# Optimization experiments

Measured on AMD Instinct MI355X. Metric: run time of the kernel, lower is better.

The kernel has to match this reference:

```python
import jax, jax.numpy as jnp
import numpy as np

H = 128  # hidden_dim


def gcn_conv(x, src, dst, n, W, b):
    """PyG GCNConv: add self-loops, symmetric norm, gather-transform-scatter."""
    h = x @ W  # [n, H]
    loop = jnp.arange(n, dtype=src.dtype)
    s = jnp.concatenate([src, loop])
    d = jnp.concatenate([dst, loop])
    deg = jax.ops.segment_sum(jnp.ones(s.shape[0], h.dtype), d, num_segments=n)
    dinv = jnp.where(deg > 0, jax.lax.rsqrt(deg), 0.0)
    norm = dinv[s] * dinv[d]  # [E+n]
    msg = h[s] * norm[:, None]
    out = jax.ops.segment_sum(msg, d, num_segments=n)
    return out + b


def encode(x, edge_index, batch, num_graphs, params):
    src, dst = edge_index[0], edge_index[1]
    n = x.shape[0]
    for (W, b) in params:
        x = jax.nn.relu(gcn_conv(x, src, dst, n, W, b))
    sums = jax.ops.segment_sum(x, batch, num_segments=num_graphs)
    cnts = jax.ops.segment_sum(jnp.ones((n, 1), x.dtype), batch, num_segments=num_graphs)
    return sums / jnp.maximum(cnts, 1.0)  # global_mean_pool -> [B, H]


def setup_inputs() -> dict:
    key = jax.random.key(0)
    ks = jax.random.split(key, 32)
    B, C = 32, 5
    Nd, Ed = 1280, 5120
    Np, Ep = 12800, 204800
    f32 = jnp.float32

    def lin(k, fan_in, fan_out):
        k1, k2 = jax.random.split(k)
        lim = 1.0 / np.sqrt(fan_in)
        W = jax.random.uniform(k1, (fan_in, fan_out), f32, -lim, lim)
        b = jax.random.uniform(k2, (fan_out,), f32, -lim, lim)
        return W, b

    Wd0, bd0 = lin(ks[0], 78, H)
    Wd1, bd1 = lin(ks[1], H, H)
    Wd2, bd2 = lin(ks[2], H, H)
    Wp0, bp0 = lin(ks[3], 1280, H)
    Wp1, bp1 = lin(ks[4], H, H)
    Wp2, bp2 = lin(ks[5], H, H)
    Wq, bq = lin(ks[6], H, H)
    Wk, bk = lin(ks[7], H, H)
    Wv, bv = lin(ks[8], H, H)
    W1, b1 = lin(ks[9], 2 * H, H)
    W2, b2 = lin(ks[10], H, 1)

    drug_x = jax.random.normal(ks[11], (Nd, 78), f32)
    prot_x = jax.random.normal(ks[12], (C, Np, 1280), f32)
    drug_edge_index = jax.random.randint(ks[13], (2, Ed), 0, Nd, jnp.int32)
    prot_edge_index = jax.random.randint(ks[14], (C, 2, Ep), 0, Np, jnp.int32)
    # equal-sized graphs per batch element -> every segment non-empty
    drug_batch = (jnp.arange(Nd, dtype=jnp.int32) * B) // Nd
    prot_batch = (jnp.arange(Np, dtype=jnp.int32) * B) // Np

    return dict(drug_x=drug_x, prot_x=prot_x,
                Wd0=Wd0, bd0=bd0, Wd1=Wd1, bd1=bd1, Wd2=Wd2, bd2=bd2,
                Wp0=Wp0, bp0=bp0, Wp1=Wp1, bp1=bp1, Wp2=Wp2, bp2=bp2,
                Wq=Wq, bq=bq, Wk=Wk, bk=bk, Wv=Wv, bv=bv,
                W1=W1, b1=b1, W2=W2, b2=b2,
                drug_edge_index=drug_edge_index, prot_edge_index=prot_edge_index,
                drug_batch=drug_batch, prot_batch=prot_batch, num_graphs=B)


def reference(drug_x, prot_x, Wd0, bd0, Wd1, bd1, Wd2, bd2,
              Wp0, bp0, Wp1, bp1, Wp2, bp2,
              Wq, bq, Wk, bk, Wv, bv, W1, b1, W2, b2,
              drug_edge_index, prot_edge_index, drug_batch, prot_batch, num_graphs):
    drug_params = [(Wd0, bd0), (Wd1, bd1), (Wd2, bd2)]
    prot_params = [(Wp0, bp0), (Wp1, bp1), (Wp2, bp2)]

    drug_emb = encode(drug_x, drug_edge_index, drug_batch, num_graphs, drug_params)  # [B,H]

    # vmap over conformations -> [C, B, H]
    conf = jax.vmap(lambda x, ei: encode(x, ei, prot_batch, num_graphs, prot_params))(
        prot_x, prot_edge_index)
    conf = jnp.transpose(conf, (1, 0, 2))  # [B, C, H]

    # drug-conditioned cross-attention over conformations
    q = drug_emb @ Wq + bq                      # [B,H]
    keys = conf @ Wk + bk                       # [B,C,H]
    vals = conf @ Wv + bv                       # [B,C,H]
    scores = jnp.einsum('bh,bch->bc', q, keys) / jnp.sqrt(jnp.asarray(H, q.dtype))
    attn = jax.nn.softmax(scores, axis=1)       # [B,C]
    protein_emb = jnp.einsum('bc,bch->bh', attn, vals)

    combined = jnp.concatenate([drug_emb, protein_emb], axis=1)  # [B,2H]
    hidden = jax.nn.relu(combined @ W1 + b1)    # dropout is identity in eval mode
    logits = (hidden @ W2 + b2)[:, 0]           # [B]
    return logits, attn
```

## Files before the change

kernel.cpp:

```cpp
#include <hip/hip_runtime.h>

#define H     128
#define BGR   32
#define NCONF 5
#define ND    1280
#define FD    78
#define ED    5120
#define NP    12800
#define FP    1280
#define EP    204800
#define MAXD  64

#define PROT_GEMM1_BLKS 1000
#define PROT_GEMM_BLKS 500
#define DRUG_GEMM1_BLKS 20
#define DRUG_GEMM_BLKS 10
#define PLACE_BLKS 4020
#define PROT_MP_BLKS 16000
#define DRUG_MP_BLKS 320

typedef unsigned short u16;
typedef unsigned int   u32;
typedef __attribute__((ext_vector_type(8))) short bf16x8;
typedef __attribute__((ext_vector_type(4))) unsigned int u32x4;
typedef __attribute__((ext_vector_type(4))) unsigned short u16x4;
typedef __attribute__((ext_vector_type(8))) unsigned short u16x8;
typedef __attribute__((ext_vector_type(4))) float f32x4;

__device__ __forceinline__ u16 f2bf(float x) {
  u32 u = __float_as_uint(x);
  u32 r = (u + 0x7FFFu + ((u >> 16) & 1u)) >> 16;
  return (u16)r;
}
__device__ __forceinline__ float bf2f(u16 h) {
  return __uint_as_float(((u32)h) << 16);
}

__device__ __forceinline__ void gload16(const void* gsrc, void* lds) {
  __builtin_amdgcn_global_load_lds(
      (const __attribute__((address_space(1))) unsigned int*)gsrc,
      (__attribute__((address_space(3))) unsigned int*)lds, 16, 0, 0);
}

__device__ __forceinline__ void cvt8(float4 p, float4 q, bf16x8& hi, bf16x8& lo) {
  float f[8] = {p.x, p.y, p.z, p.w, q.x, q.y, q.z, q.w};
  u32x4 h, l;
  #pragma unroll
  for (int j = 0; j < 4; ++j) {
    u32 u0 = __float_as_uint(f[2 * j]);
    u32 u1 = __float_as_uint(f[2 * j + 1]);
    u32 h0 = u0 & 0xFFFF0000u;
    u32 h1 = u1 & 0xFFFF0000u;
    h[j] = (h0 >> 16) | h1;
    float l0 = f[2 * j]     - __uint_as_float(h0);
    float l1 = f[2 * j + 1] - __uint_as_float(h1);
    l[j] = (__float_as_uint(l0) >> 16) | (__float_as_uint(l1) & 0xFFFF0000u);
  }
  union { u32x4 u; bf16x8 b; } ch, cl;
  ch.u = h; cl.u = l;
  hi = ch.b; lo = cl.b;
}

__device__ __forceinline__ void splitW_chunk(
    const float* __restrict__ W, u16* __restrict__ wsW, int K, int g)
{
  int step = g >> 10;
  int r = g & 1023;
  int col = r >> 3, q = r & 7;
  int u = q ^ (col & 7);
  int kc = (u & 3) * 8;
  bool lo = u >= 4;
  int k0 = step * 32 + kc;
  u16x8 o;
  #pragma unroll
  for (int j = 0; j < 8; ++j) {
    float x = W[(size_t)(k0 + j) * 128 + col];
    u16 h = f2bf(x);
    o[j] = lo ? f2bf(x - bf2f(h)) : h;
  }
  *(u16x8*)(wsW + (size_t)g * 8) = o;
}

__global__ __launch_bounds__(256) void splitW_all_k(
    const float* __restrict__ Wp0, const float* __restrict__ Wp1,
    const float* __restrict__ Wp2, const float* __restrict__ Wd1,
    const float* __restrict__ Wd2,
    u16* __restrict__ o0, u16* __restrict__ o1, u16* __restrict__ o2,
    u16* __restrict__ o3, u16* __restrict__ o4,
    int* __restrict__ deg_p, int* __restrict__ deg_d)
{
  int g = blockIdx.x * 256 + threadIdx.x;
  for (int i = g; i < NCONF * NP + ND; i += 224 * 256) {
    if (i < NCONF * NP) deg_p[i] = 0;
    else                deg_d[i - NCONF * NP] = 0;
  }
  if      (g < 40960) splitW_chunk(Wp0, o0, FP, g);
  else if (g < 45056) splitW_chunk(Wp1, o1, H, g - 40960);
  else if (g < 49152) splitW_chunk(Wp2, o2, H, g - 45056);
  else if (g < 53248) splitW_chunk(Wd1, o3, H, g - 49152);
  else if (g < 57344) splitW_chunk(Wd2, o4, H, g - 53248);
}

__device__ __forceinline__ void gemm_pipe64_body(
    char* smemRaw, const float* __restrict__ A, const u16* __restrict__ wsW,
    u16* __restrict__ Cout, int K, int blk)
{
  u16* Wlds = (u16*)smemRaw;
  const int t = threadIdx.x;
  const int wid = t >> 6, lane = t & 63;
  const int lane15 = lane & 15, lq = lane >> 4;
  const int m0 = blk * 64;
  const int NT = K >> 5;

  const float* Ar = A + (size_t)(m0 + wid * 16 + lane15) * K + lq * 8;
  const u16* sbase = wsW + (size_t)(wid * 4) * 512 + (size_t)lane * 8;

  f32x4 acc[8];
  #pragma unroll
  for (int j = 0; j < 8; ++j) acc[j] = (f32x4){0.f, 0.f, 0.f, 0.f};

  #define STAGE_W(step, buf) do {                                   \
    const u16* s_ = sbase + (size_t)(step) * 8192;                  \
    u16* d_ = &Wlds[(buf) * 8192 + wid * 2048];                     \
    gload16(s_,        d_);                                         \
    gload16(s_ + 512,  d_ + 512);                                   \
    gload16(s_ + 1024, d_ + 1024);                                  \
    gload16(s_ + 1536, d_ + 1536);                                  \
  } while (0)

  STAGE_W(0, 0);
  asm volatile("" ::: "memory");
  float4 xa0 = *(const float4*)(Ar);
  float4 xa1 = *(const float4*)(Ar + 4);
  asm volatile("" ::: "memory");
  float4 ya0 = *(const float4*)(Ar + 32);
  float4 ya1 = *(const float4*)(Ar + 36);

  #define BODY64(T, RA0, RA1) do {                                            \
    if ((T) < NT - 1) asm volatile("s_waitcnt vmcnt(2)\ns_barrier" ::: "memory"); \
    else              asm volatile("s_waitcnt vmcnt(0)\ns_barrier"  ::: "memory"); \
    if ((T) + 1 < NT) { STAGE_W((T) + 1, ((T) + 1) & 1); }                    \
    asm volatile("" ::: "memory");                                            \
    bf16x8 ah, al;                                                            \
    cvt8(RA0, RA1, ah, al);                                                   \
    if ((T) + 2 < NT) {                                                       \
      const float* p_ = Ar + (size_t)((T) + 2) * 32;                          \
      RA0 = *(const float4*)(p_); RA1 = *(const float4*)(p_ + 4);             \
    }                                                                         \
    const char* base_ = (const char*)&Wlds[((T) & 1) * 8192];                 \
    _Pragma("unroll")                                                         \
    for (int cb = 0; cb < 8; ++cb) {                                          \
      int col_ = cb * 16 + lane15;                                            \
      const char* cbp_ = base_ + col_ * 128;                                  \
      int sw_ = (col_ & 7) << 4;                                              \
      bf16x8 bh_ = *(const bf16x8*)(cbp_ + ((lq << 4) ^ sw_));                \
      bf16x8 bl_ = *(const bf16x8*)(cbp_ + (((lq | 4) << 4) ^ sw_));          \
      acc[cb] = __builtin_amdgcn_mfma_f32_16x16x32_bf16(ah, bh_, acc[cb], 0, 0, 0); \
      acc[cb] = __builtin_amdgcn_mfma_f32_16x16x32_bf16(al, bh_, acc[cb], 0, 0, 0); \
      acc[cb] = __builtin_amdgcn_mfma_f32_16x16x32_bf16(ah, bl_, acc[cb], 0, 0, 0); \
    }                                                                         \
  } while (0)

  for (int tt = 0; tt < NT; tt += 2) {
    BODY64(tt,     xa0, xa1);
    BODY64(tt + 1, ya0, ya1);
  }
  #undef BODY64
  #undef STAGE_W

  #pragma unroll
  for (int j = 0; j < 4; ++j) {
    int row = m0 + wid * 16 + lq * 4 + j;
    u16* Crow = Cout + (size_t)row * 128 + lane15;
    #pragma unroll
    for (int cb = 0; cb < 8; ++cb)
      Crow[cb * 16] = f2bf(acc[cb][j]);
  }
}

__device__ __forceinline__ void gemm_pipe_bf16A_body(
    char* smemRaw, const u16* __restrict__ A, const u16* __restrict__ wsW,
    u16* __restrict__ Cout, int K, int blk)
{
  u16* Wlds = (u16*)smemRaw;
  const int t = threadIdx.x;
  const int wid = t >> 6, lane = t & 63;
  const int lane15 = lane & 15, lq = lane >> 4;
  const int m0 = blk * 128;
  const int NT = K >> 5;

  const u16* Ar0 = A + (size_t)(m0 + wid * 32 + lane15) * K + lq * 8;
  const u16* Ar1 = Ar0 + (size_t)16 * K;
  const u16* sbase = wsW + (size_t)(wid * 4) * 512 + (size_t)lane * 8;

  f32x4 acc[2][8];
  #pragma unroll
  for (int i = 0; i < 2; ++i)
    #pragma unroll
    for (int j = 0; j < 8; ++j)
      acc[i][j] = (f32x4){0.f, 0.f, 0.f, 0.f};

  #define STAGE_W(step, buf) do {                                   \
    const u16* s_ = sbase + (size_t)(step) * 8192;                  \
    u16* d_ = &Wlds[(buf) * 8192 + wid * 2048];                     \
    gload16(s_,        d_);                                         \
    gload16(s_ + 512,  d_ + 512);                                   \
    gload16(s_ + 1024, d_ + 1024);                                  \
    gload16(s_ + 1536, d_ + 1536);                                  \
  } while (0)

  STAGE_W(0, 0);
  asm volatile("" ::: "memory");
  u16x8 xa = *(const u16x8*)(Ar0);
  u16x8 xb = *(const u16x8*)(Ar1);
  asm volatile("" ::: "memory");
  u16x8 ya = *(const u16x8*)(Ar0 + 32);
  u16x8 yb = *(const u16x8*)(Ar1 + 32);

  #define BODYB(T, RA, RB) do {                                               \
    if ((T) < NT - 1) asm volatile("s_waitcnt vmcnt(2)\ns_barrier" ::: "memory"); \
    else              asm volatile("s_waitcnt vmcnt(0)\ns_barrier"  ::: "memory"); \
    if ((T) + 1 < NT) { STAGE_W((T) + 1, ((T) + 1) & 1); }                    \
    asm volatile("" ::: "memory");                                            \
    union { u16x8 u; bf16x8 b; } ca_, cb2_;                                   \
    ca_.u = RA; cb2_.u = RB;                                                  \
    bf16x8 a0 = ca_.b, a1 = cb2_.b;                                           \
    if ((T) + 2 < NT) {                                                       \
      RA = *(const u16x8*)(Ar0 + (size_t)((T) + 2) * 32);                     \
      RB = *(const u16x8*)(Ar1 + (size_t)((T) + 2) * 32);                     \
    }                                                                         \
    const char* base_ = (const char*)&Wlds[((T) & 1) * 8192];                 \
    _Pragma("unroll")                                                         \
    for (int cb = 0; cb < 8; ++cb) {                                          \
      int col_ = cb * 16 + lane15;                                            \
      const char* cbp_ = base_ + col_ * 128;                                  \
      int sw_ = (col_ & 7) << 4;                                              \
      bf16x8 bh_ = *(const bf16x8*)(cbp_ + ((lq << 4) ^ sw_));                \
      bf16x8 bl_ = *(const bf16x8*)(cbp_ + (((lq | 4) << 4) ^ sw_));          \
      acc[0][cb] = __builtin_amdgcn_mfma_f32_16x16x32_bf16(a0, bh_, acc[0][cb], 0, 0, 0); \
      acc[0][cb] = __builtin_amdgcn_mfma_f32_16x16x32_bf16(a0, bl_, acc[0][cb], 0, 0, 0); \
      acc[1][cb] = __builtin_amdgcn_mfma_f32_16x16x32_bf16(a1, bh_, acc[1][cb], 0, 0, 0); \
      acc[1][cb] = __builtin_amdgcn_mfma_f32_16x16x32_bf16(a1, bl_, acc[1][cb], 0, 0, 0); \
    }                                                                         \
  } while (0)

  for (int tt = 0; tt < NT; tt += 2) {
    BODYB(tt,     xa, xb);
    BODYB(tt + 1, ya, yb);
  }
  #undef BODYB
  #undef STAGE_W

  #pragma unroll
  for (int rb = 0; rb < 2; ++rb) {
    #pragma unroll
    for (int j = 0; j < 4; ++j) {
      int row = m0 + wid * 32 + rb * 16 + lq * 4 + j;
      u16* Crow = Cout + (size_t)row * 128 + lane15;
      #pragma unroll
      for (int cb = 0; cb < 8; ++cb)
        Crow[cb * 16] = f2bf(acc[rb][cb][j]);
    }
  }
}

__device__ __forceinline__ void gemm_f32_body(
    char* smemRaw, const float* __restrict__ A, const float* __restrict__ W,
    u16* __restrict__ Cout, int K, int blk)
{
  float* As = (float*)smemRaw;
  float* Bs = (float*)(smemRaw + 16 * 64 * 4);
  const int t = threadIdx.x;
  const int m0 = blk * 64;
  const int colg = (t & 31) * 4;
  const int rowg = (t >> 5) * 8;
  const int rA = t >> 2;
  const int cA = (t & 3) * 4;
  const int rB = t >> 4;
  const int cB = (t & 15) * 4;

  float acc[8][4] = {};

  for (int k0 = 0; k0 < K; k0 += 16) {
    __syncthreads();
    #pragma unroll
    for (int j = 0; j < 4; ++j) {
      int kk = k0 + cA + j;
      As[(cA + j) * 64 + rA] = (kk < K) ? A[(size_t)(m0 + rA) * K + kk] : 0.0f;
    }
    {
      int kk = k0 + rB;
      if (kk < K) {
        *(float4*)&Bs[rB * 128 + cB]      = *(const float4*)(W + (size_t)kk * 128 + cB);
        *(float4*)&Bs[rB * 128 + cB + 64] = *(const float4*)(W + (size_t)kk * 128 + cB + 64);
      } else {
        *(float4*)&Bs[rB * 128 + cB]      = make_float4(0.f, 0.f, 0.f, 0.f);
        *(float4*)&Bs[rB * 128 + cB + 64] = make_float4(0.f, 0.f, 0.f, 0.f);
      }
    }
    __syncthreads();
    #pragma unroll
    for (int k = 0; k < 16; ++k) {
      float4 b  = *(const float4*)&Bs[k * 128 + colg];
      float4 a0 = *(const float4*)&As[k * 64 + rowg];
      float4 a1 = *(const float4*)&As[k * 64 + rowg + 4];
      const float av[8] = {a0.x, a0.y, a0.z, a0.w, a1.x, a1.y, a1.z, a1.w};
      #pragma unroll
      for (int i = 0; i < 8; ++i) {
        acc[i][0] += av[i] * b.x;
        acc[i][1] += av[i] * b.y;
        acc[i][2] += av[i] * b.z;
        acc[i][3] += av[i] * b.w;
      }
    }
  }
  #pragma unroll
  for (int i = 0; i < 8; ++i) {
    u16x4 o;
    o[0] = f2bf(acc[i][0]); o[1] = f2bf(acc[i][1]);
    o[2] = f2bf(acc[i][2]); o[3] = f2bf(acc[i][3]);
    *(u16x4*)(Cout + (size_t)(m0 + rowg + i) * 128 + colg) = o;
  }
}

__global__ __launch_bounds__(256, 4) void stage1_place_k(
    const float* __restrict__ pA, const u16* __restrict__ pW, u16* __restrict__ pC,
    const float* __restrict__ dA, const float* __restrict__ dW, u16* __restrict__ dC,
    const int* __restrict__ prot_ei, const int* __restrict__ drug_ei,
    int* __restrict__ deg_p, u16* __restrict__ slot_p,
    int* __restrict__ deg_d, u16* __restrict__ slot_d)
{
  __shared__ __align__(16) char smem[2 * 16384];
  int b = blockIdx.x;
  if (b < PROT_GEMM1_BLKS) {
    gemm_pipe64_body(smem, pA, pW, pC, FP, b);
    return;
  }
  b -= PROT_GEMM1_BLKS;
  if (b < DRUG_GEMM1_BLKS) {
    gemm_f32_body(smem, dA, dW, dC, FD, b);
    return;
  }
  b -= DRUG_GEMM1_BLKS;
  int idx = b * 256 + threadIdx.x;
  if (idx < NCONF * EP) {
    int c = idx / EP, e = idx - c * EP;
    const int* eic = prot_ei + (size_t)c * 2 * EP;
    int s = eic[e], d = eic[EP + e];
    int node = c * NP + d;
    int pos = atomicAdd(&deg_p[node], 1);
    if (pos < MAXD) slot_p[(size_t)node * MAXD + pos] = (u16)s;
  } else {
    idx -= NCONF * EP;
    if (idx < ED) {
      int s = drug_ei[idx], d = drug_ei[ED + idx];
      int pos = atomicAdd(&deg_d[d], 1);
      if (pos < MAXD) slot_d[(size_t)d * MAXD + pos] = (u16)s;
    }
  }
}

__global__ __launch_bounds__(256, 4) void stage23_gemm_k(
    const u16* __restrict__ pA, const u16* __restrict__ pW, u16* __restrict__ pC,
    const u16* __restrict__ dA, const u16* __restrict__ dW, u16* __restrict__ dC)
{
  __shared__ __align__(16) char smem[2 * 16384];
  if (blockIdx.x < PROT_GEMM_BLKS)
    gemm_pipe_bf16A_body(smem, pA, pW, pC, H, blockIdx.x);
  else
    gemm_pipe_bf16A_body(smem, dA, dW, dC, H, blockIdx.x - PROT_GEMM_BLKS);
}

__device__ __forceinline__ void mp_body(
    const u16* __restrict__ h, u16* __restrict__ xout,
    const int* __restrict__ deg, const u16* __restrict__ slots,
    const float* __restrict__ bias, int wid, int nPer)
{
  int lane = threadIdx.x & 63;
  int c = wid / nPer;
  const int* dg = deg + (size_t)c * nPer;
  int v = wid - c * nPer;
  const u32* hc = (const u32*)(h + (size_t)c * nPer * H);
  const u16* sl = slots + (size_t)wid * MAXD;
  int degv = dg[v];
  float dv = rsqrtf((float)degv + 1.0f);
  u32 us = ((const u32*)h)[(size_t)wid * 64 + lane];
  float a0x = __uint_as_float(us << 16) * dv;
  float a0y = __uint_as_float(us & 0xFFFF0000u) * dv;
  float a1x = 0.f, a1y = 0.f;
  int n = degv < MAXD ? degv : MAXD;
  int i = 0;
  for (; i + 4 <= n; i += 4) {
    int s0 = sl[i], s1 = sl[i + 1], s2 = sl[i + 2], s3 = sl[i + 3];
    float d0 = rsqrtf((float)dg[s0] + 1.0f);
    float d1 = rsqrtf((float)dg[s1] + 1.0f);
    float d2 = rsqrtf((float)dg[s2] + 1.0f);
    float d3 = rsqrtf((float)dg[s3] + 1.0f);
    u32 u0 = hc[(size_t)s0 * 64 + lane];
    u32 u1 = hc[(size_t)s1 * 64 + lane];
    u32 u2 = hc[(size_t)s2 * 64 + lane];
    u32 u3 = hc[(size_t)s3 * 64 + lane];
    a0x += __uint_as_float(u0 << 16) * d0;
    a0y += __uint_as_float(u0 & 0xFFFF0000u) * d0;
    a1x += __uint_as_float(u1 << 16) * d1;
    a1y += __uint_as_float(u1 & 0xFFFF0000u) * d1;
    a0x += __uint_as_float(u2 << 16) * d2;
    a0y += __uint_as_float(u2 & 0xFFFF0000u) * d2;
    a1x += __uint_as_float(u3 << 16) * d3;
    a1y += __uint_as_float(u3 & 0xFFFF0000u) * d3;
  }
  for (; i < n; ++i) {
    int s0 = sl[i];
    float d0 = rsqrtf((float)dg[s0] + 1.0f);
    u32 u0 = hc[(size_t)s0 * 64 + lane];
    a0x += __uint_as_float(u0 << 16) * d0;
    a0y += __uint_as_float(u0 & 0xFFFF0000u) * d0;
  }
  int col = lane * 2;
  float ox = fmaxf((a0x + a1x) * dv + bias[col],     0.0f);
  float oy = fmaxf((a0y + a1y) * dv + bias[col + 1], 0.0f);
  u32 ow = (u32)f2bf(ox) | ((u32)f2bf(oy) << 16);
  ((u32*)xout)[(size_t)wid * 64 + lane] = ow;
}

__global__ __launch_bounds__(256) void mp_all_k(
    const u16* __restrict__ hp, u16* __restrict__ xp,
    const int* __restrict__ degp, const u16* __restrict__ slotp,
    const float* __restrict__ biasp,
    const u16* __restrict__ hd, u16* __restrict__ xd,
    const int* __restrict__ degd, const u16* __restrict__ slotd,
    const float* __restrict__ biasd)
{
  int bid = blockIdx.x;
  int cpx = gridDim.x >> 3;
  bid = (bid & 7) * cpx + (bid >> 3);
  int wv = threadIdx.x >> 6;
  if (bid < PROT_MP_BLKS) {
    mp_body(hp, xp, degp, slotp, biasp, bid * 4 + wv, NP);
  } else {
    mp_body(hd, xd, degd, slotd, biasd, (bid - PROT_MP_BLKS) * 4 + wv, ND);
  }
}

__device__ __forceinline__ void pool_body(
    const u16* __restrict__ x, float* __restrict__ out, int blk, int npg)
{
  __shared__ float part[4][128];
  const int col = threadIdx.x & 127;
  const int rp  = threadIdx.x >> 7;
  size_t row0 = (size_t)blk * npg;
  float acc = 0.0f;
  for (int i = rp; i < npg; i += 4)
    acc += bf2f(x[(row0 + i) * H + col]);
  part[rp][col] = acc;
  __syncthreads();
  if (rp == 0)
    out[(size_t)blk * H + col] =
        (part[0][col] + part[1][col] + part[2][col] + part[3][col]) / (float)npg;
}

__global__ __launch_bounds__(512) void pool_all_k(
    const u16* __restrict__ xd, float* __restrict__ outd,
    const u16* __restrict__ xp, float* __restrict__ outp)
{
  if (blockIdx.x < BGR) pool_body(xd, outd, blockIdx.x, ND / BGR);
  else                  pool_body(xp, outp, blockIdx.x - BGR, NP / BGR);
}

__global__ __launch_bounds__(128) void attn_mlp_k(
    const float* __restrict__ drug_emb, const float* __restrict__ conf_pool,
    const float* __restrict__ Wq, const float* __restrict__ bq,
    const float* __restrict__ Wk, const float* __restrict__ bk,
    const float* __restrict__ Wv, const float* __restrict__ bv,
    const float* __restrict__ W1, const float* __restrict__ b1,
    const float* __restrict__ W2, const float* __restrict__ b2,
    float* __restrict__ out)
{
  const int b = blockIdx.x;
  const int hcol = threadIdx.x;
  __shared__ float de[H], pc[H], vals_s[NCONF][H], red[H], sc[NCONF], peS[H];

  de[hcol] = drug_emb[(size_t)b * H + hcol];
  __syncthreads();

  float qv = bq[hcol];
  for (int k = 0; k < H; ++k) qv += de[k] * Wq[k * H + hcol];

  for (int c = 0; c < NCONF; ++c) {
    __syncthreads();
    pc[hcol] = conf_pool[((size_t)c * BGR + b) * H + hcol];
    __syncthreads();
    float kk = bk[hcol], vv = bv[hcol];
    for (int k = 0; k < H; ++k) {
      float p = pc[k];
      kk += p * Wk[k * H + hcol];
      vv += p * Wv[k * H + hcol];
    }
    vals_s[c][hcol] = vv;
    red[hcol] = qv * kk;
    __syncthreads();
    for (int s = 64; s > 0; s >>= 1) {
      if (hcol < s) red[hcol] += red[hcol + s];
      __syncthreads();
    }
    if (hcol == 0) sc[c] = red[0] * 0.08838834764831845f;
  }
  __syncthreads();

  float m = sc[0];
  for (int c = 1; c < NCONF; ++c) m = fmaxf(m, sc[c]);
  float ex[NCONF], sum = 0.0f;
  for (int c = 0; c < NCONF; ++c) { ex[c] = expf(sc[c] - m); sum += ex[c]; }
  float inv = 1.0f / sum;
  if (hcol < NCONF) out[BGR + b * NCONF + hcol] = ex[hcol] * inv;

  float pe = 0.0f;
  for (int c = 0; c < NCONF; ++c) pe += (ex[c] * inv) * vals_s[c][hcol];
  peS[hcol] = pe;
  __syncthreads();

  float hid = b1[hcol];
  for (int k = 0; k < H; ++k) hid += de[k]  * W1[k * H + hcol];
  for (int k = 0; k < H; ++k) hid += peS[k] * W1[(H + k) * H + hcol];
  hid = fmaxf(hid, 0.0f);

  red[hcol] = hid * W2[hcol];
  __syncthreads();
  for (int s = 64; s > 0; s >>= 1) {
    if (hcol < s) red[hcol] += red[hcol + s];
    __syncthreads();
  }
  if (hcol == 0) out[b] = red[0] + b2[0];
}

extern "C" void kernel_launch(void* const* d_in, const int* in_sizes, int n_in,
                              void* d_out, int out_size, void* d_ws, size_t ws_size,
                              hipStream_t stream)
{
  const float* drug_x  = (const float*)d_in[0];
  const float* prot_x  = (const float*)d_in[1];
  const float* Wd0 = (const float*)d_in[2];  const float* bd0 = (const float*)d_in[3];
  const float* Wd1 = (const float*)d_in[4];  const float* bd1 = (const float*)d_in[5];
  const float* Wd2 = (const float*)d_in[6];  const float* bd2 = (const float*)d_in[7];
  const float* Wp0 = (const float*)d_in[8];  const float* bp0 = (const float*)d_in[9];
  const float* Wp1 = (const float*)d_in[10]; const float* bp1 = (const float*)d_in[11];
  const float* Wp2 = (const float*)d_in[12]; const float* bp2 = (const float*)d_in[13];
  const float* Wq  = (const float*)d_in[14]; const float* bq  = (const float*)d_in[15];
  const float* Wk  = (const float*)d_in[16]; const float* bk  = (const float*)d_in[17];
  const float* Wv  = (const float*)d_in[18]; const float* bv  = (const float*)d_in[19];
  const float* W1  = (const float*)d_in[20]; const float* b1  = (const float*)d_in[21];
  const float* W2  = (const float*)d_in[22]; const float* b2  = (const float*)d_in[23];
  const int* drug_ei = (const int*)d_in[24];
  const int* prot_ei = (const int*)d_in[25];
  float* out = (float*)d_out;

  char* base = (char*)d_ws;
  size_t off = 0;
  auto alloc = [&](size_t bytes) -> char* {
    char* p = base + off;
    off = (off + bytes + 255) & ~(size_t)255;
    return p;
  };
  int*   deg_p   = (int*)  alloc((size_t)NCONF * NP * 4);
  int*   deg_d   = (int*)  alloc((size_t)ND * 4);
  u16*   slot_p  = (u16*)  alloc((size_t)NCONF * NP * MAXD * 2);
  u16*   slot_d  = (u16*)  alloc((size_t)ND * MAXD * 2);
  u16*   bufHp   = (u16*)  alloc((size_t)NCONF * NP * H * 2);
  u16*   bufXp   = (u16*)  alloc((size_t)NCONF * NP * H * 2);
  u16*   bufHd   = (u16*)  alloc((size_t)ND * H * 2);
  u16*   bufXd   = (u16*)  alloc((size_t)ND * H * 2);
  float* drugemb = (float*)alloc((size_t)BGR * H * 4);
  float* confp   = (float*)alloc((size_t)NCONF * BGR * H * 4);
  u16* Wp0ws = (u16*)alloc((size_t)FP * 512);
  u16* Wp1ws = (u16*)alloc((size_t)H * 512);
  u16* Wp2ws = (u16*)alloc((size_t)H * 512);
  u16* Wd1ws = (u16*)alloc((size_t)H * 512);
  u16* Wd2ws = (u16*)alloc((size_t)H * 512);

  splitW_all_k<<<224, 256, 0, stream>>>(Wp0, Wp1, Wp2, Wd1, Wd2,
                                        Wp0ws, Wp1ws, Wp2ws, Wd1ws, Wd2ws,
                                        deg_p, deg_d);

  stage1_place_k<<<PROT_GEMM1_BLKS + DRUG_GEMM1_BLKS + PLACE_BLKS, 256, 0, stream>>>(
      prot_x, Wp0ws, bufHp, drug_x, Wd0, bufHd,
      prot_ei, drug_ei, deg_p, slot_p, deg_d, slot_d);

  mp_all_k<<<PROT_MP_BLKS + DRUG_MP_BLKS, 256, 0, stream>>>(
      bufHp, bufXp, deg_p, slot_p, bp0,
      bufHd, bufXd, deg_d, slot_d, bd0);
  stage23_gemm_k<<<PROT_GEMM_BLKS + DRUG_GEMM_BLKS, 256, 0, stream>>>(
      bufXp, Wp1ws, bufHp, bufXd, Wd1ws, bufHd);
  mp_all_k<<<PROT_MP_BLKS + DRUG_MP_BLKS, 256, 0, stream>>>(
      bufHp, bufXp, deg_p, slot_p, bp1,
      bufHd, bufXd, deg_d, slot_d, bd1);
  stage23_gemm_k<<<PROT_GEMM_BLKS + DRUG_GEMM_BLKS, 256, 0, stream>>>(
      bufXp, Wp2ws, bufHp, bufXd, Wd2ws, bufHd);
  mp_all_k<<<PROT_MP_BLKS + DRUG_MP_BLKS, 256, 0, stream>>>(
      bufHp, bufXp, deg_p, slot_p, bp2,
      bufHd, bufXd, deg_d, slot_d, bd2);

  pool_all_k<<<BGR + NCONF * BGR, 512, 0, stream>>>(bufXd, drugemb, bufXp, confp);

  attn_mlp_k<<<BGR, 128, 0, stream>>>(drugemb, confp, Wq, bq, Wk, bk, Wv, bv,
                                      W1, b1, W2, b2, out);
}
```

Before: 371.5 us.

## Process four nodes per wavefront with 16-byte gathers in message passing

Message passing now assigns 16 lanes to each destination node, so one wavefront handles four nodes. Each lane gathers 8 bf16 features with a single 16-byte load instead of 4 bytes. Neighbor indices and their normalization factors are loaded in parallel across the 16 lanes and broadcast with shuffles, with 8 neighbor rows loaded at once for more memory-level parallelism. The grid shrinks fourfold. It adds per-lane register pressure, and nodes of different degree now share a wavefront, which can cause divergence.

```diff
diff --git a/kernel.cpp b/kernel.cpp
--- a/kernel.cpp
+++ b/kernel.cpp
@@ -16,8 +16,8 @@
 #define DRUG_GEMM1_BLKS 20
 #define DRUG_GEMM_BLKS 10
 #define PLACE_BLKS 4020
-#define PROT_MP_BLKS 16000
-#define DRUG_MP_BLKS 320
+#define PROT_MP4_BLKS 4000
+#define DRUG_MP4_BLKS 80
 
 typedef unsigned short u16;
 typedef unsigned int   u32;
@@ -371,56 +371,70 @@
     gemm_pipe_bf16A_body(smem, dA, dW, dC, H, blockIdx.x - PROT_GEMM_BLKS);
 }
 
-__device__ __forceinline__ void mp_body(
+__device__ __forceinline__ void mp_body4(
     const u16* __restrict__ h, u16* __restrict__ xout,
     const int* __restrict__ deg, const u16* __restrict__ slots,
-    const float* __restrict__ bias, int wid, int nPer)
-{
-  int lane = threadIdx.x & 63;
-  int c = wid / nPer;
+    const float* __restrict__ bias, int nodeBase, int nPer)
+{
+  const int lane = threadIdx.x & 63;
+  const int lane16 = lane & 15;
+  const int grp = lane >> 4;
+  const int wv = threadIdx.x >> 6;
+  const int node = nodeBase + wv * 4 + grp;
+  const int c = node / nPer;
+  const int v = node - c * nPer;
   const int* dg = deg + (size_t)c * nPer;
-  int v = wid - c * nPer;
-  const u32* hc = (const u32*)(h + (size_t)c * nPer * H);
-  const u16* sl = slots + (size_t)wid * MAXD;
-  int degv = dg[v];
-  float dv = rsqrtf((float)degv + 1.0f);
-  u32 us = ((const u32*)h)[(size_t)wid * 64 + lane];
-  float a0x = __uint_as_float(us << 16) * dv;
-  float a0y = __uint_as_float(us & 0xFFFF0000u) * dv;
-  float a1x = 0.f, a1y = 0.f;
-  int n = degv < MAXD ? degv : MAXD;
-  int i = 0;
-  for (; i + 4 <= n; i += 4) {
-    int s0 = sl[i], s1 = sl[i + 1], s2 = sl[i + 2], s3 = sl[i + 3];
-    float d0 = rsqrtf((float)dg[s0] + 1.0f);
-    float d1 = rsqrtf((float)dg[s1] + 1.0f);
-    float d2 = rsqrtf((float)dg[s2] + 1.0f);
-    float d3 = rsqrtf((float)dg[s3] + 1.0f);
-    u32 u0 = hc[(size_t)s0 * 64 + lane];
-    u32 u1 = hc[(size_t)s1 * 64 + lane];
-    u32 u2 = hc[(size_t)s2 * 64 + lane];
-    u32 u3 = hc[(size_t)s3 * 64 + lane];
-    a0x += __uint_as_float(u0 << 16) * d0;
-    a0y += __uint_as_float(u0 & 0xFFFF0000u) * d0;
-    a1x += __uint_as_float(u1 << 16) * d1;
-    a1y += __uint_as_float(u1 & 0xFFFF0000u) * d1;
-    a0x += __uint_as_float(u2 << 16) * d2;
-    a0y += __uint_as_float(u2 & 0xFFFF0000u) * d2;
-    a1x += __uint_as_float(u3 << 16) * d3;
-    a1y += __uint_as_float(u3 & 0xFFFF0000u) * d3;
-  }
-  for (; i < n; ++i) {
-    int s0 = sl[i];
-    float d0 = rsqrtf((float)dg[s0] + 1.0f);
-    u32 u0 = hc[(size_t)s0 * 64 + lane];
-    a0x += __uint_as_float(u0 << 16) * d0;
-    a0y += __uint_as_float(u0 & 0xFFFF0000u) * d0;
-  }
-  int col = lane * 2;
-  float ox = fmaxf((a0x + a1x) * dv + bias[col],     0.0f);
-  float oy = fmaxf((a0y + a1y) * dv + bias[col + 1], 0.0f);
-  u32 ow = (u32)f2bf(ox) | ((u32)f2bf(oy) << 16);
-  ((u32*)xout)[(size_t)wid * 64 + lane] = ow;
+  const u16* hc = h + (size_t)c * nPer * H;
+  const u16* sl = slots + (size_t)node * MAXD;
+  const int degv = dg[v];
+  const float dv = rsqrtf((float)degv + 1.0f);
+  const int n = degv < MAXD ? degv : MAXD;
+
+  u16x8 selfv = *(const u16x8*)(hc + (size_t)v * H + lane16 * 8);
+  float acc[8];
+  #pragma unroll
+  for (int q = 0; q < 8; ++q) acc[q] = bf2f(selfv[q]) * dv;
+
+  for (int base = 0; base < n; base += 16) {
+    int m = n - base; if (m > 16) m = 16;
+    int sj = (lane16 < m) ? (int)sl[base + lane16] : 0;
+    float dj = (lane16 < m) ? rsqrtf((float)dg[sj] + 1.0f) : 0.0f;
+    int i = 0;
+    for (; i + 8 <= m; i += 8) {
+      int s_[8]; float d_[8]; u16x8 u_[8];
+      #pragma unroll
+      for (int j = 0; j < 8; ++j) {
+        s_[j] = __shfl(sj, (grp << 4) | (i + j));
+        d_[j] = __shfl(dj, (grp << 4) | (i + j));
+      }
+      #pragma unroll
+      for (int j = 0; j < 8; ++j)
+        u_[j] = *(const u16x8*)(hc + (size_t)s_[j] * H + lane16 * 8);
+      #pragma unroll
+      for (int j = 0; j < 8; ++j) {
+        #pragma unroll
+        for (int q = 0; q < 8; ++q)
+          acc[q] += bf2f(u_[j][q]) * d_[j];
+      }
+    }
+    for (; i < m; ++i) {
+      int s0 = __shfl(sj, (grp << 4) | i);
+      float d0 = __shfl(dj, (grp << 4) | i);
+      u16x8 u0 = *(const u16x8*)(hc + (size_t)s0 * H + lane16 * 8);
+      #pragma unroll
+      for (int q = 0; q < 8; ++q)
+        acc[q] += bf2f(u0[q]) * d0;
+    }
+  }
+
+  const int col0 = lane16 * 8;
+  u16x8 o;
+  #pragma unroll
+  for (int q = 0; q < 8; ++q) {
+    float x = fmaxf(acc[q] * dv + bias[col0 + q], 0.0f);
+    o[q] = f2bf(x);
+  }
+  *(u16x8*)(xout + (size_t)node * H + col0) = o;
 }
 
 __global__ __launch_bounds__(256) void mp_all_k(
@@ -434,11 +448,10 @@
   int bid = blockIdx.x;
   int cpx = gridDim.x >> 3;
   bid = (bid & 7) * cpx + (bid >> 3);
-  int wv = threadIdx.x >> 6;
-  if (bid < PROT_MP_BLKS) {
-    mp_body(hp, xp, degp, slotp, biasp, bid * 4 + wv, NP);
+  if (bid < PROT_MP4_BLKS) {
+    mp_body4(hp, xp, degp, slotp, biasp, bid * 16, NP);
   } else {
-    mp_body(hd, xd, degd, slotd, biasd, (bid - PROT_MP_BLKS) * 4 + wv, ND);
+    mp_body4(hd, xd, degd, slotd, biasd, (bid - PROT_MP4_BLKS) * 16, ND);
   }
 }
 
@@ -585,17 +598,17 @@
       prot_x, Wp0ws, bufHp, drug_x, Wd0, bufHd,
       prot_ei, drug_ei, deg_p, slot_p, deg_d, slot_d);
 
-  mp_all_k<<<PROT_MP_BLKS + DRUG_MP_BLKS, 256, 0, stream>>>(
+  mp_all_k<<<PROT_MP4_BLKS + DRUG_MP4_BLKS, 256, 0, stream>>>(
       bufHp, bufXp, deg_p, slot_p, bp0,
       bufHd, bufXd, deg_d, slot_d, bd0);
   stage23_gemm_k<<<PROT_GEMM_BLKS + DRUG_GEMM_BLKS, 256, 0, stream>>>(
       bufXp, Wp1ws, bufHp, bufXd, Wd1ws, bufHd);
-  mp_all_k<<<PROT_MP_BLKS + DRUG_MP_BLKS, 256, 0, stream>>>(
+  mp_all_k<<<PROT_MP4_BLKS + DRUG_MP4_BLKS, 256, 0, stream>>>(
       bufHp, bufXp, deg_p, slot_p, bp1,
       bufHd, bufXd, deg_d, slot_d, bd1);
   stage23_gemm_k<<<PROT_GEMM_BLKS + DRUG_GEMM_BLKS, 256, 0, stream>>>(
       bufXp, Wp2ws, bufHp, bufXd, Wd2ws, bufHd);
-  mp_all_k<<<PROT_MP_BLKS + DRUG_MP_BLKS, 256, 0, stream>>>(
+  mp_all_k<<<PROT_MP4_BLKS + DRUG_MP4_BLKS, 256, 0, stream>>>(
       bufHp, bufXp, deg_p, slot_p, bp2,
       bufHd, bufXd, deg_d, slot_d, bd2);
 
```

Result: faster. 346.2 us (-6.8%).
